# Performance work log

Hardware: AMD Instinct MI355X
Metric: run time of the kernel (lower is better)

The kernel has to match this reference:

```python
import jax, jax.numpy as jnp
import numpy as np

B, S, D = 2, 2048, 2048
H, KV, HD = 32, 8, 64
REP = H // KV  # 4


def setup_inputs() -> dict:
    key = jax.random.key(0)
    ks = jax.random.split(key, 5)
    x = jax.random.normal(ks[0], (B, S, D), jnp.float32)
    # Llama rope frequencies: theta=10000, pairs of adjacent dims
    inv_freq = 1.0 / (10000.0 ** (np.arange(0, HD, 2, dtype=np.float64) / HD))  # [HD/2]
    ang = np.outer(np.arange(S, dtype=np.float64), inv_freq)  # [S, HD/2]
    freqs_cis = jnp.asarray(np.stack([np.cos(ang), np.sin(ang)], axis=-1), jnp.float32)  # [S, HD/2, 2]
    wq = jax.random.normal(ks[1], (H * HD, D), jnp.float32) * 0.02
    wk = jax.random.normal(ks[2], (KV * HD, D), jnp.float32) * 0.02
    wv = jax.random.normal(ks[3], (KV * HD, D), jnp.float32) * 0.02
    wo = jax.random.normal(ks[4], (D, H * HD), jnp.float32) * 0.02
    return {"x": x, "freqs_cis": freqs_cis, "wq": wq, "wk": wk, "wv": wv, "wo": wo}


def _apply_rope(t, cos, sin):
    # t: [B,S,nh,HD]; cos/sin: [S,HD/2]; complex multiply on adjacent pairs
    b, s, nh, hd = t.shape
    t2 = t.reshape(b, s, nh, hd // 2, 2)
    tr, ti = t2[..., 0], t2[..., 1]
    c = cos[None, :, None, :]
    sn = sin[None, :, None, :]
    out = jnp.stack([tr * c - ti * sn, tr * sn + ti * c], axis=-1)
    return out.reshape(b, s, nh, hd)


def reference(x, freqs_cis, wq, wk, wv, wo):
    # QKV projections (torch Linear: y = x @ W.T)
    q = jnp.einsum('bsd,ed->bse', x, wq).reshape(B, S, H, HD)
    k = jnp.einsum('bsd,ed->bse', x, wk).reshape(B, S, KV, HD)
    v = jnp.einsum('bsd,ed->bse', x, wv).reshape(B, S, KV, HD)
    cos, sin = freqs_cis[..., 0], freqs_cis[..., 1]
    q = _apply_rope(q, cos, sin)
    k = _apply_rope(k, cos, sin)
    # GQA without materializing repeated K/V: group query heads by KV head
    qg = q.reshape(B, S, KV, REP, HD)
    scale = 1.0 / jnp.sqrt(jnp.asarray(HD, q.dtype))
    scores = jnp.einsum('bsgrd,btgd->bgrst', qg, k) * scale  # [B,KV,REP,S,S]
    causal = jnp.tril(jnp.ones((S, S), bool))
    scores = jnp.where(causal, scores, -jnp.inf)
    p = jax.nn.softmax(scores, axis=-1)
    o = jnp.einsum('bgrst,btgd->bsgrd', p, v).reshape(B, S, H * HD)
    return jnp.einsum('bse,de->bsd', o, wo)
```

## Files before the change

### kernel.cpp

```cpp
#include <hip/hip_runtime.h>
#include <cstdint>
#include <cstddef>

#define B_ 2
#define S_ 2048
#define D_ 2048
#define H_ 32
#define KV_ 8
#define HD_ 64
#define M_ (B_*S_)
#define EQ_ (H_*HD_)
#define EK_ (KV_*HD_)

typedef unsigned short u16;
typedef __attribute__((ext_vector_type(8))) short s16x8;
typedef __attribute__((ext_vector_type(4))) float f32x4;

#define QSCALE 0.18033688011112042f
#define EXPOFF 15.869645449778564f

#if __has_builtin(__builtin_amdgcn_exp2f)
#define EXP2(x) __builtin_amdgcn_exp2f(x)
#else
#define EXP2(x) __expf((x) * 0.6931471805599453f)
#endif

__device__ __forceinline__ u16 f2bf(float f) {
  unsigned u = __float_as_uint(f);
  u += 0x7fffu + ((u >> 16) & 1u);
  return (u16)(u >> 16);
}
__device__ __forceinline__ unsigned pk2(float a, float b) {
  unsigned ua = __float_as_uint(a) + 0x8000u;
  unsigned ub = __float_as_uint(b) + 0x8000u;
  return __builtin_amdgcn_perm(ub, ua, 0x07060302);
}
__device__ __forceinline__ f32x4 mfma16(s16x8 a, s16x8 b, f32x4 c) {
  return __builtin_amdgcn_mfma_f32_16x16x32_bf16(a, b, c, 0, 0, 0);
}
__device__ __forceinline__ void gl_lds16(const void* g, void* l) {
  __builtin_amdgcn_global_load_lds(
      (const __attribute__((address_space(1))) void*)g,
      (__attribute__((address_space(3))) void*)l, 16, 0, 0);
}

__global__ void cast_all(const float4* __restrict__ x, const float4* __restrict__ wq,
                         const float4* __restrict__ wk, const float4* __restrict__ wv,
                         const float4* __restrict__ wo, ushort4* __restrict__ dst) {
  int i = blockIdx.x * 256 + threadIdx.x;
  const float4* src; int off;
  if (i < 2097152)      { src = x;  off = i; }
  else if (i < 3145728) { src = wq; off = i - 2097152; }
  else if (i < 3407872) { src = wk; off = i - 3145728; }
  else if (i < 3670016) { src = wv; off = i - 3407872; }
  else                  { src = wo; off = i - 3670016; }
  float4 v = src[off];
  ushort4 r;
  r.x = f2bf(v.x); r.y = f2bf(v.y); r.z = f2bf(v.z); r.w = f2bf(v.w);
  dst[i] = r;
}

__global__ __launch_bounds__(256)
void gemm_qkv(const u16* __restrict__ A, const u16* __restrict__ Bw,
              u16* __restrict__ qb, u16* __restrict__ kb, u16* __restrict__ vtb,
              const float* __restrict__ fc) {
  __shared__ __align__(16) u16 As[128 * 64];
  __shared__ __align__(16) u16 Bs[128 * 64];
  const int tid  = threadIdx.x;
  const int lane = tid & 63;
  const int wave = tid >> 6;
  const int m0 = blockIdx.y * 128;
  const int n0 = blockIdx.x * 128;
  const int wm = (wave >> 1) * 64;
  const int wn = (wave & 1) * 64;
  const int l15 = lane & 15;
  const int quad = lane >> 4;

  f32x4 acc[4][4] = {};

  for (int k0 = 0; k0 < D_; k0 += 64) {
    #pragma unroll
    for (int rr = 0; rr < 4; ++rr) {
      int c = tid + rr * 256;
      int row = c >> 3;
      int ksrc = ((c & 7) ^ (row & 7)) * 8;
      gl_lds16(A  + (size_t)(m0 + row) * D_ + k0 + ksrc, &As[c * 8]);
      gl_lds16(Bw + (size_t)(n0 + row) * D_ + k0 + ksrc, &Bs[c * 8]);
    }
    __syncthreads();

    #pragma unroll
    for (int kc = 0; kc < 2; ++kc) {
      s16x8 af[4], bfr[4];
      #pragma unroll
      for (int mi = 0; mi < 4; ++mi) {
        int row = wm + mi * 16 + l15;
        af[mi]  = *(const s16x8*)&As[row * 64 + (((kc * 4 + quad) ^ (row & 7)) * 8)];
      }
      #pragma unroll
      for (int ni = 0; ni < 4; ++ni) {
        int row = wn + ni * 16 + l15;
        bfr[ni] = *(const s16x8*)&Bs[row * 64 + (((kc * 4 + quad) ^ (row & 7)) * 8)];
      }
      #pragma unroll
      for (int mi = 0; mi < 4; ++mi)
        #pragma unroll
        for (int ni = 0; ni < 4; ++ni)
          acc[mi][ni] = mfma16(af[mi], bfr[ni], acc[mi][ni]);
    }
    __syncthreads();
  }

  if (n0 < 2560) {
    const bool isQ = (n0 < 2048);
    u16* dst = isQ ? qb : kb;
    const int ncol0 = isQ ? 0 : 2048;
    const int ndim  = isQ ? EQ_ : EK_;
    const float scale = isQ ? QSCALE : 1.0f;
    const float sg = (l15 & 1) ? 1.f : -1.f;
    #pragma unroll
    for (int mi = 0; mi < 4; ++mi) {
      #pragma unroll
      for (int r = 0; r < 4; ++r) {
        int row = m0 + wm + mi * 16 + quad * 4 + r;
        const float* fr = fc + (size_t)(row & (S_ - 1)) * 64;
        #pragma unroll
        for (int ni = 0; ni < 4; ++ni) {
          int col = n0 + wn + ni * 16 + l15;
          int ip = (col & 63) >> 1;
          float c  = fr[ip * 2];
          float sn = fr[ip * 2 + 1];
          float v = acc[mi][ni][r];
          float p = __shfl_xor(v, 1, 64);
          float o = (v * c + sg * (p * sn)) * scale;
          dst[(size_t)row * ndim + col - ncol0] = f2bf(o);
        }
      }
    }
  } else {
    #pragma unroll
    for (int mi = 0; mi < 4; ++mi) {
      #pragma unroll
      for (int ni = 0; ni < 4; ++ni) {
        int vcol = n0 + wn + ni * 16 + l15 - 2560;
        uint2 w;
        w.x = pk2(acc[mi][ni][0], acc[mi][ni][1]);
        w.y = pk2(acc[mi][ni][2], acc[mi][ni][3]);
        *(uint2*)(vtb + (size_t)vcol * M_ + m0 + wm + mi * 16 + quad * 4) = w;
      }
    }
  }
}

__global__ __launch_bounds__(256)
void gemm_o(const u16* __restrict__ A, const u16* __restrict__ Bw, float* __restrict__ C,
            int Ndim, int Kdim) {
  __shared__ __align__(16) u16 As[128 * 64];
  __shared__ __align__(16) u16 Bs[64 * 64];
  const int tid  = threadIdx.x;
  const int lane = tid & 63;
  const int wave = tid >> 6;
  const int m0 = blockIdx.y * 128;
  const int n0 = blockIdx.x * 64;
  const int wm = (wave >> 1) * 64;
  const int wn = (wave & 1) * 32;
  const int l15 = lane & 15;
  const int quad = lane >> 4;

  f32x4 acc[4][2] = {};

  for (int k0 = 0; k0 < Kdim; k0 += 64) {
    #pragma unroll
    for (int rr = 0; rr < 4; ++rr) {
      int c = tid + rr * 256;
      int row = c >> 3;
      int ksrc = ((c & 7) ^ (row & 7)) * 8;
      gl_lds16(A + (size_t)(m0 + row) * Kdim + k0 + ksrc, &As[c * 8]);
    }
    #pragma unroll
    for (int rr = 0; rr < 2; ++rr) {
      int c = tid + rr * 256;
      int row = c >> 3;
      int ksrc = ((c & 7) ^ (row & 7)) * 8;
      gl_lds16(Bw + (size_t)(n0 + row) * Kdim + k0 + ksrc, &Bs[c * 8]);
    }
    __syncthreads();

    #pragma unroll
    for (int kc = 0; kc < 2; ++kc) {
      s16x8 af[4], bfr[2];
      #pragma unroll
      for (int mi = 0; mi < 4; ++mi) {
        int row = wm + mi * 16 + l15;
        af[mi]  = *(const s16x8*)&As[row * 64 + (((kc * 4 + quad) ^ (row & 7)) * 8)];
      }
      #pragma unroll
      for (int ni = 0; ni < 2; ++ni) {
        int row = wn + ni * 16 + l15;
        bfr[ni] = *(const s16x8*)&Bs[row * 64 + (((kc * 4 + quad) ^ (row & 7)) * 8)];
      }
      #pragma unroll
      for (int mi = 0; mi < 4; ++mi)
        #pragma unroll
        for (int ni = 0; ni < 2; ++ni)
          acc[mi][ni] = mfma16(af[mi], bfr[ni], acc[mi][ni]);
    }
    __syncthreads();
  }

  #pragma unroll
  for (int mi = 0; mi < 4; ++mi) {
    #pragma unroll
    for (int r = 0; r < 4; ++r) {
      int row = m0 + wm + mi * 16 + quad * 4 + r;
      size_t base = (size_t)row * Ndim + n0 + wn;
      #pragma unroll
      for (int ni = 0; ni < 2; ++ni)
        C[base + ni * 16 + l15] = acc[mi][ni][r];
    }
  }
}

__global__ __launch_bounds__(256, 4)
void flash_attn(const u16* __restrict__ qb, const u16* __restrict__ kb,
                const u16* __restrict__ vtb, u16* __restrict__ ob) {
  const int bx = blockIdx.x;
  const int h  = blockIdx.y;
  const int b  = blockIdx.z;
  const int g  = h >> 2;
  const int tid  = threadIdx.x;
  const int lane = tid & 63;
  const int wave = tid >> 6;
  const int l15  = lane & 15;
  const int quad = lane >> 4;
  const int kq   = quad * 8;

  const int Tlo = bx, Thi = 31 - bx;
  const int n_lo = Tlo + 1, n_hi = Thi + 1;
  const int rL = Tlo * 64 + wave * 16;
  const int rH = Thi * 64 + wave * 16;
  const int rowL = rL + l15;
  const int rowH = rH + l15;

  __shared__ __align__(16) u16 Ks[8 * 512];
  __shared__ __align__(16) u16 Vs[8 * 512];
  __shared__ __align__(16) u16 Pl[4][2][16 * 72];

  u16* PbL = &Pl[wave][0][0];
  u16* PbH = &Pl[wave][1][0];

  const u16* qpL = qb + (size_t)(b * S_ + rL + l15) * EQ_ + h * HD_;
  const u16* qpH = qb + (size_t)(b * S_ + rH + l15) * EQ_ + h * HD_;
  s16x8 qL0 = *(const s16x8*)(qpL + kq);
  s16x8 qL1 = *(const s16x8*)(qpL + 32 + kq);
  s16x8 qH0 = *(const s16x8*)(qpH + kq);
  s16x8 qH1 = *(const s16x8*)(qpH + 32 + kq);

  f32x4 OL[4] = {}, OH[4] = {};
  float sumL = 0.f, sumH = 0.f;

  const int sw = wave & 1;
  const bool doK = (wave < 2);

  for (int kt = 0; kt < n_hi; ++kt) {
    const int t0 = kt * 64;

    if (doK) {
      const u16* src = kb + (size_t)(b * S_ + t0 + lane) * EK_ + g * HD_;
      #pragma unroll
      for (int r = 0; r < 4; ++r) {
        int i = sw * 4 + r;
        gl_lds16(src + i * 8, &Ks[i * 512 + lane * 8]);
      }
    } else {
      const u16* src = vtb + (size_t)(g * HD_ + lane) * M_ + b * S_ + t0;
      #pragma unroll
      for (int r = 0; r < 4; ++r) {
        int i = sw * 4 + r;
        gl_lds16(src + i * 8, &Vs[i * 512 + lane * 8]);
      }
    }
    __syncthreads();

    const bool do_lo = (kt < n_lo);
    const bool mH = (kt == n_hi - 1);
    const bool mL = (kt == n_lo - 1);

    #pragma unroll
    for (int ts = 0; ts < 4; ++ts) {
      s16x8 k0 = *(const s16x8*)&Ks[quad * 512 + (ts * 16 + l15) * 8];
      s16x8 k1 = *(const s16x8*)&Ks[(4 + quad) * 512 + (ts * 16 + l15) * 8];
      const int tb = t0 + ts * 16 + quad * 4;
      {
        f32x4 s = {};
        s = mfma16(k0, qH0, s);
        s = mfma16(k1, qH1, s);
        if (mH) {
          #pragma unroll
          for (int r = 0; r < 4; ++r) if (tb + r > rowH) s[r] = -1e30f;
        }
        float p0 = EXP2(s[0] - EXPOFF), p1 = EXP2(s[1] - EXPOFF);
        float p2 = EXP2(s[2] - EXPOFF), p3 = EXP2(s[3] - EXPOFF);
        sumH += (p0 + p1) + (p2 + p3);
        uint2 w; w.x = pk2(p0, p1); w.y = pk2(p2, p3);
        *(uint2*)&PbH[l15 * 72 + ts * 16 + quad * 4] = w;
      }
      if (do_lo) {
        f32x4 s = {};
        s = mfma16(k0, qL0, s);
        s = mfma16(k1, qL1, s);
        if (mL) {
          #pragma unroll
          for (int r = 0; r < 4; ++r) if (tb + r > rowL) s[r] = -1e30f;
        }
        float p0 = EXP2(s[0] - EXPOFF), p1 = EXP2(s[1] - EXPOFF);
        float p2 = EXP2(s[2] - EXPOFF), p3 = EXP2(s[3] - EXPOFF);
        sumL += (p0 + p1) + (p2 + p3);
        uint2 w; w.x = pk2(p0, p1); w.y = pk2(p2, p3);
        *(uint2*)&PbL[l15 * 72 + ts * 16 + quad * 4] = w;
      }
    }

    s16x8 pH0 = *(const s16x8*)&PbH[l15 * 72 + kq];
    s16x8 pH1 = *(const s16x8*)&PbH[l15 * 72 + 32 + kq];
    s16x8 pL0 = {}, pL1 = {};
    if (do_lo) {
      pL0 = *(const s16x8*)&PbL[l15 * 72 + kq];
      pL1 = *(const s16x8*)&PbL[l15 * 72 + 32 + kq];
    }

    #pragma unroll
    for (int df = 0; df < 4; ++df) {
      s16x8 v0 = *(const s16x8*)&Vs[quad * 512 + (df * 16 + l15) * 8];
      s16x8 v1 = *(const s16x8*)&Vs[(4 + quad) * 512 + (df * 16 + l15) * 8];
      OH[df] = mfma16(v1, pH1, mfma16(v0, pH0, OH[df]));
      if (do_lo) OL[df] = mfma16(v1, pL1, mfma16(v0, pL0, OL[df]));
    }
    __syncthreads();
  }

  sumH += __shfl_xor(sumH, 16, 64); sumH += __shfl_xor(sumH, 32, 64);
  sumL += __shfl_xor(sumL, 16, 64); sumL += __shfl_xor(sumL, 32, 64);
  float invH = 1.f / sumH, invL = 1.f / sumL;

  {
    u16* op = ob + (size_t)(b * S_ + rowH) * EQ_ + h * HD_;
    #pragma unroll
    for (int df = 0; df < 4; ++df) {
      uint2 w;
      w.x = pk2(OH[df][0] * invH, OH[df][1] * invH);
      w.y = pk2(OH[df][2] * invH, OH[df][3] * invH);
      *(uint2*)(op + df * 16 + quad * 4) = w;
    }
  }
  {
    u16* op = ob + (size_t)(b * S_ + rowL) * EQ_ + h * HD_;
    #pragma unroll
    for (int df = 0; df < 4; ++df) {
      uint2 w;
      w.x = pk2(OL[df][0] * invL, OL[df][1] * invL);
      w.y = pk2(OL[df][2] * invL, OL[df][3] * invL);
      *(uint2*)(op + df * 16 + quad * 4) = w;
    }
  }
}

extern "C" void kernel_launch(void* const* d_in, const int* in_sizes, int n_in,
                              void* d_out, int out_size, void* d_ws, size_t ws_size,
                              hipStream_t stream) {
  (void)in_sizes; (void)n_in; (void)out_size; (void)ws_size;
  const float* x  = (const float*)d_in[0];
  const float* fc = (const float*)d_in[1];
  const float* wq = (const float*)d_in[2];
  const float* wk = (const float*)d_in[3];
  const float* wv = (const float*)d_in[4];
  const float* wo = (const float*)d_in[5];
  float* out = (float*)d_out;
  char* ws = (char*)d_ws;

  u16* xb  = (u16*)(ws);
  u16* wqb = (u16*)(ws + 16777216);
  u16* wob = (u16*)(ws + 29360128);
  u16* qb  = (u16*)(ws + 37748736);
  u16* kb  = (u16*)(ws + 54525952);
  u16* vtb = (u16*)(ws + 58720256);
  u16* ob  = (u16*)(ws + 62914560);

  cast_all<<<18432, 256, 0, stream>>>((const float4*)x, (const float4*)wq,
                                      (const float4*)wk, (const float4*)wv,
                                      (const float4*)wo, (ushort4*)ws);

  gemm_qkv<<<dim3(24, 32), 256, 0, stream>>>(xb, wqb, qb, kb, vtb, fc);

  flash_attn<<<dim3(16, 32, 2), 256, 0, stream>>>(qb, kb, vtb, ob);

  gemm_o<<<dim3(32, 32), 256, 0, stream>>>(ob, wob, out, D_, EQ_);
}
```

Measured before the change: 316.8 us.

## Widen output GEMM tile to 128x128 and restructure flash attention schedule

The output projection GEMM now uses 512-thread blocks with a 128x128 tile, so fewer blocks each reuse the A tile across more columns. The flash attention kernel is reorganised: K fragments are read directly from global memory instead of being staged in LDS. The 33 key tiles of a paired low/high query block are split across two wave groups, each working on its own V buffer, so lo and hi tiles are processed in separate visits rather than interleaved. This removes idle lo-branch work and K LDS traffic, at the cost of uncoalesced global K loads and each wave loading its own K data.

```diff
diff --git a/kernel.cpp b/kernel.cpp
--- a/kernel.cpp
+++ b/kernel.cpp
@@ -152,18 +152,18 @@
   }
 }
 
-__global__ __launch_bounds__(256)
+__global__ __launch_bounds__(512)
 void gemm_o(const u16* __restrict__ A, const u16* __restrict__ Bw, float* __restrict__ C,
             int Ndim, int Kdim) {
   __shared__ __align__(16) u16 As[128 * 64];
-  __shared__ __align__(16) u16 Bs[64 * 64];
+  __shared__ __align__(16) u16 Bs[128 * 64];
   const int tid  = threadIdx.x;
   const int lane = tid & 63;
   const int wave = tid >> 6;
   const int m0 = blockIdx.y * 128;
-  const int n0 = blockIdx.x * 64;
-  const int wm = (wave >> 1) * 64;
-  const int wn = (wave & 1) * 32;
+  const int n0 = blockIdx.x * 128;
+  const int wm = (wave >> 2) * 64;
+  const int wn = (wave & 3) * 32;
   const int l15 = lane & 15;
   const int quad = lane >> 4;
 
@@ -171,17 +171,11 @@
 
   for (int k0 = 0; k0 < Kdim; k0 += 64) {
     #pragma unroll
-    for (int rr = 0; rr < 4; ++rr) {
-      int c = tid + rr * 256;
+    for (int rr = 0; rr < 2; ++rr) {
+      int c = tid + rr * 512;
       int row = c >> 3;
       int ksrc = ((c & 7) ^ (row & 7)) * 8;
-      gl_lds16(A + (size_t)(m0 + row) * Kdim + k0 + ksrc, &As[c * 8]);
-    }
-    #pragma unroll
-    for (int rr = 0; rr < 2; ++rr) {
-      int c = tid + rr * 256;
-      int row = c >> 3;
-      int ksrc = ((c & 7) ^ (row & 7)) * 8;
+      gl_lds16(A  + (size_t)(m0 + row) * Kdim + k0 + ksrc, &As[c * 8]);
       gl_lds16(Bw + (size_t)(n0 + row) * Kdim + k0 + ksrc, &Bs[c * 8]);
     }
     __syncthreads();
@@ -236,18 +230,17 @@
   const int kq   = quad * 8;
 
   const int Tlo = bx, Thi = 31 - bx;
-  const int n_lo = Tlo + 1, n_hi = Thi + 1;
+  const int n_lo = Tlo + 1;
   const int rL = Tlo * 64 + wave * 16;
   const int rH = Thi * 64 + wave * 16;
   const int rowL = rL + l15;
   const int rowH = rH + l15;
 
-  __shared__ __align__(16) u16 Ks[8 * 512];
-  __shared__ __align__(16) u16 Vs[8 * 512];
-  __shared__ __align__(16) u16 Pl[4][2][16 * 72];
-
-  u16* PbL = &Pl[wave][0][0];
-  u16* PbH = &Pl[wave][1][0];
+  __shared__ __align__(16) u16 Vs[2][8 * 512];
+  __shared__ __align__(16) u16 Pl[4][16 * 72];
+
+  const u16* kbg  = kb  + (size_t)b * S_ * EK_ + g * HD_;
+  const u16* vtbg = vtb + ((size_t)(g * HD_ + lane)) * M_ + b * S_;
 
   const u16* qpL = qb + (size_t)(b * S_ + rL + l15) * EQ_ + h * HD_;
   const u16* qpH = qb + (size_t)(b * S_ + rH + l15) * EQ_ + h * HD_;
@@ -258,83 +251,70 @@
 
   f32x4 OL[4] = {}, OH[4] = {};
   float sumL = 0.f, sumH = 0.f;
-
-  const int sw = wave & 1;
-  const bool doK = (wave < 2);
-
-  for (int kt = 0; kt < n_hi; ++kt) {
+  u16* pw = &Pl[wave][0];
+
+  auto visit = [&](int kt, bool msk, const s16x8& qa0, const s16x8& qa1,
+                   int qrow, f32x4* O, float& sum, const u16* Vsl) {
     const int t0 = kt * 64;
-
-    if (doK) {
-      const u16* src = kb + (size_t)(b * S_ + t0 + lane) * EK_ + g * HD_;
-      #pragma unroll
-      for (int r = 0; r < 4; ++r) {
-        int i = sw * 4 + r;
-        gl_lds16(src + i * 8, &Ks[i * 512 + lane * 8]);
-      }
-    } else {
-      const u16* src = vtb + (size_t)(g * HD_ + lane) * M_ + b * S_ + t0;
-      #pragma unroll
-      for (int r = 0; r < 4; ++r) {
-        int i = sw * 4 + r;
-        gl_lds16(src + i * 8, &Vs[i * 512 + lane * 8]);
-      }
-    }
-    __syncthreads();
-
-    const bool do_lo = (kt < n_lo);
-    const bool mH = (kt == n_hi - 1);
-    const bool mL = (kt == n_lo - 1);
-
+    f32x4 sc[4];
     #pragma unroll
     for (int ts = 0; ts < 4; ++ts) {
-      s16x8 k0 = *(const s16x8*)&Ks[quad * 512 + (ts * 16 + l15) * 8];
-      s16x8 k1 = *(const s16x8*)&Ks[(4 + quad) * 512 + (ts * 16 + l15) * 8];
-      const int tb = t0 + ts * 16 + quad * 4;
-      {
-        f32x4 s = {};
-        s = mfma16(k0, qH0, s);
-        s = mfma16(k1, qH1, s);
-        if (mH) {
-          #pragma unroll
-          for (int r = 0; r < 4; ++r) if (tb + r > rowH) s[r] = -1e30f;
+      const u16* kp = kbg + (size_t)(t0 + ts * 16 + l15) * EK_;
+      s16x8 k0 = *(const s16x8*)(kp + kq);
+      s16x8 k1 = *(const s16x8*)(kp + 32 + kq);
+      f32x4 s = {};
+      s = mfma16(k0, qa0, s);
+      sc[ts] = mfma16(k1, qa1, s);
+    }
+    #pragma unroll
+    for (int ts = 0; ts < 4; ++ts) {
+      f32x4 s = sc[ts];
+      if (msk) {
+        const int tb = t0 + ts * 16 + quad * 4;
+        #pragma unroll
+        for (int r = 0; r < 4; ++r) if (tb + r > qrow) s[r] = -1e30f;
+      }
+      float p0 = EXP2(s[0] - EXPOFF), p1 = EXP2(s[1] - EXPOFF);
+      float p2 = EXP2(s[2] - EXPOFF), p3 = EXP2(s[3] - EXPOFF);
+      sum += (p0 + p1) + (p2 + p3);
+      uint2 w; w.x = pk2(p0, p1); w.y = pk2(p2, p3);
+      *(uint2*)&pw[l15 * 72 + ts * 16 + quad * 4] = w;
+    }
+    s16x8 pa0 = *(const s16x8*)&pw[l15 * 72 + kq];
+    s16x8 pa1 = *(const s16x8*)&pw[l15 * 72 + 32 + kq];
+    #pragma unroll
+    for (int df = 0; df < 4; ++df) {
+      s16x8 v0 = *(const s16x8*)&Vsl[quad * 512 + (df * 16 + l15) * 8];
+      s16x8 v1 = *(const s16x8*)&Vsl[(4 + quad) * 512 + (df * 16 + l15) * 8];
+      O[df] = mfma16(v1, pa1, mfma16(v0, pa0, O[df]));
+    }
+  };
+
+  for (int rd = 0; rd < 17; ++rd) {
+    {
+      const int gs = (wave >> 1) * 17 + rd;
+      if (gs < 33) {
+        const int rg = (gs >= n_lo) ? 1 : 0;
+        const int kt = rg ? gs - n_lo : gs;
+        const u16* src = vtbg + kt * 64;
+        #pragma unroll
+        for (int r = 0; r < 4; ++r) {
+          int i = (wave & 1) * 4 + r;
+          gl_lds16(src + i * 8, &Vs[wave >> 1][i * 512 + lane * 8]);
         }
-        float p0 = EXP2(s[0] - EXPOFF), p1 = EXP2(s[1] - EXPOFF);
-        float p2 = EXP2(s[2] - EXPOFF), p3 = EXP2(s[3] - EXPOFF);
-        sumH += (p0 + p1) + (p2 + p3);
-        uint2 w; w.x = pk2(p0, p1); w.y = pk2(p2, p3);
-        *(uint2*)&PbH[l15 * 72 + ts * 16 + quad * 4] = w;
-      }
-      if (do_lo) {
-        f32x4 s = {};
-        s = mfma16(k0, qL0, s);
-        s = mfma16(k1, qL1, s);
-        if (mL) {
-          #pragma unroll
-          for (int r = 0; r < 4; ++r) if (tb + r > rowL) s[r] = -1e30f;
-        }
-        float p0 = EXP2(s[0] - EXPOFF), p1 = EXP2(s[1] - EXPOFF);
-        float p2 = EXP2(s[2] - EXPOFF), p3 = EXP2(s[3] - EXPOFF);
-        sumL += (p0 + p1) + (p2 + p3);
-        uint2 w; w.x = pk2(p0, p1); w.y = pk2(p2, p3);
-        *(uint2*)&PbL[l15 * 72 + ts * 16 + quad * 4] = w;
-      }
-    }
-
-    s16x8 pH0 = *(const s16x8*)&PbH[l15 * 72 + kq];
-    s16x8 pH1 = *(const s16x8*)&PbH[l15 * 72 + 32 + kq];
-    s16x8 pL0 = {}, pL1 = {};
-    if (do_lo) {
-      pL0 = *(const s16x8*)&PbL[l15 * 72 + kq];
-      pL1 = *(const s16x8*)&PbL[l15 * 72 + 32 + kq];
-    }
-
-    #pragma unroll
-    for (int df = 0; df < 4; ++df) {
-      s16x8 v0 = *(const s16x8*)&Vs[quad * 512 + (df * 16 + l15) * 8];
-      s16x8 v1 = *(const s16x8*)&Vs[(4 + quad) * 512 + (df * 16 + l15) * 8];
-      OH[df] = mfma16(v1, pH1, mfma16(v0, pH0, OH[df]));
-      if (do_lo) OL[df] = mfma16(v1, pL1, mfma16(v0, pL0, OL[df]));
+      }
+    }
+    __syncthreads();
+
+    if (rd < n_lo) visit(rd,        rd == Tlo,          qL0, qL1, rowL, OL, sumL, &Vs[0][0]);
+    else           visit(rd - n_lo, rd - n_lo == Thi,   qH0, qH1, rowH, OH, sumH, &Vs[0][0]);
+
+    {
+      const int gv = 17 + rd;
+      if (gv < 33) {
+        const int kt = gv - n_lo;
+        visit(kt, kt == Thi, qH0, qH1, rowH, OH, sumH, &Vs[1][0]);
+      }
     }
     __syncthreads();
   }
@@ -394,5 +374,5 @@
 
   flash_attn<<<dim3(16, 32, 2), 256, 0, stream>>>(qb, kb, vtb, ob);
 
-  gemm_o<<<dim3(32, 32), 256, 0, stream>>>(ob, wob, out, D_, EQ_);
-}
+  gemm_o<<<dim3(16, 32), 512, 0, stream>>>(ob, wob, out, D_, EQ_);
+}
```

New measurement: 385.9 us. 21.8% more time.
